# Performance work log

Measured on AMD Instinct MI355X. Metric: run time of the kernel, lower is better.

## Reference

```python
import jax, jax.numpy as jnp
import numpy as np


def setup_inputs() -> dict:
    key = jax.random.key(0)
    T, TOK, D = 16, 4096, 2048
    C = D // 2          # comp_dim
    H = 2 * C           # MLP hidden = comp_dim * 2
    K = 16              # comp_len
    NN = T * (TOK // 2)  # node rows == edge rows == 32768
    ks = jax.random.split(key, 10)
    x = jax.random.normal(ks[0], (T, TOK, D), dtype=jnp.float32)
    # structured ragged layout: first half of tokens are nodes, second half edges
    padded_node_mask = jnp.zeros((T, TOK), dtype=bool).at[:, :TOK // 2].set(True)
    padded_edge_mask = jnp.logical_not(padded_node_mask)
    rand_indices = jax.random.randint(ks[1], (2 * K, 1000), 0, NN)
    s = 0.02
    node_W1 = s * jax.random.normal(ks[2], (K, D, H), dtype=jnp.float32)
    node_b1 = jnp.zeros((K, H), dtype=jnp.float32)
    node_W2 = s * jax.random.normal(ks[3], (K, H, C), dtype=jnp.float32)
    node_b2 = jnp.zeros((K, C), dtype=jnp.float32)
    edge_W1 = s * jax.random.normal(ks[4], (K, D, H), dtype=jnp.float32)
    edge_b1 = jnp.zeros((K, H), dtype=jnp.float32)
    edge_W2 = s * jax.random.normal(ks[5], (K, H, C), dtype=jnp.float32)
    edge_b2 = jnp.zeros((K, C), dtype=jnp.float32)
    return {"x": x, "padded_node_mask": padded_node_mask,
            "padded_edge_mask": padded_edge_mask, "rand_indices": rand_indices,
            "node_W1": node_W1, "node_b1": node_b1, "node_W2": node_W2, "node_b2": node_b2,
            "edge_W1": edge_W1, "edge_b1": edge_b1, "edge_W2": edge_W2, "edge_b2": edge_b2}


def _branch(rows, seg, idx, W1, b1, W2, b2, T, TOK, NROWS, C):
    # rows: [NROWS, D] gathered tokens; seg: [NROWS] timestamp id per row
    # idx:  [K, 1000] sampled rows per component MLP
    sel = rows[idx]                                                # [K,1000,D]
    h = jax.nn.gelu(jnp.einsum('kld,kdh->klh', sel, W1) + b1[:, None, :],
                    approximate=False)
    h = jnp.einsum('klh,khc->klc', h, W2) + b2[:, None, :]         # [K,1000,C]

    def step(carry, args):
        i, hh = args
        # scatter-set dedupes duplicate sampled indices (same value anyway),
        # matching torch's zeros[...] = mlp(...) assignment semantics
        z = jnp.zeros((NROWS, C), dtype=hh.dtype).at[i].set(hh)    # sparse rows
        pooled = jax.ops.segment_sum(z, seg, num_segments=T)       # [T,C]
        return carry, pooled

    _, pooled = jax.lax.scan(step, None, (idx, h))                 # [K,T,C]
    # adaptive_avg_pool1d(..., 1) == mean over the full token dim (incl. zeros)
    return pooled / TOK


def reference(x, padded_node_mask, padded_edge_mask, rand_indices,
              node_W1, node_b1, node_W2, node_b2,
              edge_W1, edge_b1, edge_W2, edge_b2):
    T, TOK, D = x.shape
    C = D // 2
    K = node_W1.shape[0]
    NN = T * TOK // 2  # node rows (== edge rows for our structured masks)
    nt, ntok = jnp.nonzero(padded_node_mask, size=NN)
    et, etok = jnp.nonzero(padded_edge_mask, size=NN)
    nodes = x[nt, ntok]  # [NN, D], row-major order like torch x[mask]
    edges = x[et, etok]
    node_pooled = _branch(nodes, nt, rand_indices[:K],
                          node_W1, node_b1, node_W2, node_b2, T, TOK, NN, C)
    edge_pooled = _branch(edges, et, rand_indices[K:],
                          edge_W1, edge_b1, edge_W2, edge_b2, T, TOK, NN, C)
    comp = jnp.concatenate([node_pooled, edge_pooled], axis=0)     # [2K,T,C]
    # cat along feature dim in component order -> [T, 1, 2K*C]
    compressed_x = comp.transpose(1, 0, 2).reshape(T, 1, 2 * K * C)
    return compressed_x
```

## Files before the change

kernel.cpp:

```cpp
#include <hip/hip_runtime.h>
#include <math.h>


typedef __attribute__((ext_vector_type(8))) short bf16x8;
typedef __attribute__((ext_vector_type(4))) short s16x4;
typedef __attribute__((ext_vector_type(4))) float f32x4;
typedef unsigned int u32;

constexpr int TT    = 16;
constexpr int TOKN  = 4096;
constexpr int DD    = 2048;
constexpr int HH    = 2048;
constexpr int CC    = 1024;
constexpr int LL    = 1000;
constexpr int NCOMP = 32;
constexpr int MP    = 1024;
constexpr int BMX = 256, BNX = 128;
constexpr int MTX  = MP / BMX;
constexpr int NT1 = HH / BNX;
constexpr int NT2 = CC / BNX;
constexpr int NT  = 2048 / 64;

__device__ __forceinline__ short f2bf(float f) {
  __bf16 h = (__bf16)f;
  return *reinterpret_cast<short*>(&h);
}
__device__ __forceinline__ int swz(int row) {
  return (row & 7) ^ ((row >> 3) & 7);
}
__device__ __forceinline__ int sw(int row, int gran) {
  return (row << 6) + ((gran ^ swz(row)) << 3);
}
__device__ __forceinline__ void gl_lds16(const void* g, void* l) {
  __builtin_amdgcn_global_load_lds(
      (const __attribute__((address_space(1))) u32*)g,
      (__attribute__((address_space(3))) u32*)l, 16, 0, 0);
}

__global__ void dedup_kernel(const int* __restrict__ ridx,
                             unsigned* __restrict__ bitmap,
                             float* __restrict__ keepf) {
  int comp = blockIdx.x;
  for (int l = threadIdx.x; l < MP; l += 256) {
    float kv = 0.0f;
    if (l < LL) {
      int r = ridx[comp * LL + l];
      unsigned bit = 1u << (r & 31);
      unsigned old = atomicOr(&bitmap[(comp << 10) + (r >> 5)], bit);
      kv = (old & bit) ? 0.0f : 1.0f;
    }
    keepf[(comp << 10) + l] = kv;
  }
}

__global__ __launch_bounds__(256) void gather_kernel(
    const float* __restrict__ x, const int* __restrict__ ridx,
    short* __restrict__ Ab) {
  int bid = blockIdx.x;
  int comp = bid >> 7, rgrp = bid & 127;
  int t = threadIdx.x;
  int tr = t >> 5, tn = t & 31;
  int m = rgrp * 8 + tr;
  int mi = m < LL ? m : LL - 1;
  int r = ridx[comp * LL + mi];
  int tokoff = comp >= 16 ? TOKN / 2 : 0;
  const float* src = x + ((size_t)(r >> 11) * TOKN + (r & 2047) + tokoff) * DD;
  short* drow = Ab + ((size_t)(comp * MP + m)) * DD;
  int s_m = swz(m);
#pragma unroll
  for (int i = 0; i < 8; ++i) {
    int gi = tn + 32 * i;
    float4 f0 = *reinterpret_cast<const float4*>(src + gi * 8);
    float4 f1 = *reinterpret_cast<const float4*>(src + gi * 8 + 4);
    bf16x8 pk;
    pk[0]=f2bf(f0.x); pk[1]=f2bf(f0.y); pk[2]=f2bf(f0.z); pk[3]=f2bf(f0.w);
    pk[4]=f2bf(f1.x); pk[5]=f2bf(f1.y); pk[6]=f2bf(f1.z); pk[7]=f2bf(f1.w);
    int c = gi >> 3, g = gi & 7;
    *reinterpret_cast<bf16x8*>(&drow[c * 64 + ((g ^ s_m) << 3)]) = pk;
  }
}

template<int LDW>
__device__ __forceinline__ void kloop(
    const short* __restrict__ aBase,
    const float* __restrict__ wBase,
    short* sm, f32x4 (&acc)[8][4],
    int wm, int wn, int lr, int lg, int tid) {
  const short* aSrc0 = aBase + (size_t)(tid >> 3) * 2048 + (tid & 7) * 8;
  int ldsA0 = tid * 8;
  int tn = tid & 31, tkb = tid >> 5, bn0 = tn * 4;
  const float* wCol = wBase + bn0;

  float4 brB[8];

  auto aglds = [&](int t, int buf) {
    short* l = sm + buf * 16384;
#pragma unroll
    for (int q = 0; q < 8; ++q)
      gl_lds16(aSrc0 + (size_t)q * 65536 + t * 64, l + ldsA0 + q * 2048);
  };
  auto bload = [&](int t) {
    const float* bb = wCol + (size_t)(t * 64 + tkb * 8) * LDW;
#pragma unroll
    for (int i = 0; i < 8; ++i)
      brB[i] = *reinterpret_cast<const float4*>(bb + (size_t)i * LDW);
  };
  auto bwrite = [&]() {
    short* Bs = sm + 32768;
#pragma unroll
    for (int j = 0; j < 4; ++j) {
      bf16x8 pk;
#pragma unroll
      for (int i = 0; i < 8; ++i) pk[i] = f2bf((&brB[i].x)[j]);
      *reinterpret_cast<bf16x8*>(&Bs[sw(bn0 + j, tkb)]) = pk;
    }
  };
  auto compute = [&](int d) {
    const short* A = sm + d * 16384;
    const short* B = sm + 32768;
#pragma unroll
    for (int kk = 0; kk < 2; ++kk) {
      bf16x8 af[8], bfr[4];
#pragma unroll
      for (int i = 0; i < 8; ++i)
        af[i] = *reinterpret_cast<const bf16x8*>(&A[sw(wm + i * 16 + lr, kk * 4 + lg)]);
#pragma unroll
      for (int j = 0; j < 4; ++j)
        bfr[j] = *reinterpret_cast<const bf16x8*>(&B[sw(wn + j * 16 + lr, kk * 4 + lg)]);
      __builtin_amdgcn_s_setprio(1);
#pragma unroll
      for (int i = 0; i < 8; ++i)
#pragma unroll
        for (int j = 0; j < 4; ++j)
          acc[i][j] = __builtin_amdgcn_mfma_f32_16x16x32_bf16(af[i], bfr[j], acc[i][j], 0, 0, 0);
      __builtin_amdgcn_s_setprio(0);
    }
  };

  bload(0);
  aglds(0, 0);
  bwrite();
  bload(1);
  aglds(1, 1);
  asm volatile("s_waitcnt lgkmcnt(0)" ::: "memory");
  __builtin_amdgcn_s_barrier();

#pragma unroll 1
  for (int t = 0; t < NT; ++t) {
    if (t < NT - 1) {
      asm volatile("s_waitcnt vmcnt(16)" ::: "memory");
    } else {
      asm volatile("s_waitcnt vmcnt(0)" ::: "memory");
    }
    __builtin_amdgcn_sched_barrier(0);
    compute(t & 1);
    __builtin_amdgcn_s_barrier();
    if (t + 1 < NT) {
      bwrite();
      if (t + 2 < NT) {
        bload(t + 2);
        aglds(t + 2, t & 1);
      }
      asm volatile("s_waitcnt lgkmcnt(0)" ::: "memory");
      __builtin_amdgcn_s_barrier();
    }
  }
}

__global__ __launch_bounds__(256, 2) void gemm1_kernel(
    const float* __restrict__ nW1, const float* __restrict__ nb1,
    const float* __restrict__ eW1, const float* __restrict__ eb1,
    const short* __restrict__ Ab, short* __restrict__ hbuf) {
  __shared__ short smem[40960];

  constexpr int NWG = NCOMP * MTX * NT1;
  constexpr int CPX = NWG / 8;
  int b0 = blockIdx.x;
  int lb = (b0 & 7) * CPX + (b0 >> 3);
  int comp = lb / (MTX * NT1);
  int rem  = lb % (MTX * NT1);
  int mt = rem / NT1, nt = rem % NT1;
  bool isEdge = comp >= 16;
  int k16 = isEdge ? comp - 16 : comp;
  const float* W1 = (isEdge ? eW1 : nW1) + (size_t)k16 * DD * HH;
  const float* b1 = (isEdge ? eb1 : nb1) + (size_t)k16 * HH;

  int tid = threadIdx.x, lane = tid & 63, wid = tid >> 6;
  int wm = (wid >> 1) << 7, wn = (wid & 1) << 6;
  int lr = lane & 15, lg = lane >> 4;

  f32x4 acc[8][4] = {};
  kloop<HH>(Ab + ((size_t)(comp * MP + mt * BMX)) * DD,
            W1 + nt * BNX, smem, acc, wm, wn, lr, lg, tid);

  __builtin_amdgcn_s_barrier();
  short* Cs = smem;
  const float* b1p = b1 + nt * BNX;
#pragma unroll
  for (int i = 0; i < 8; ++i)
#pragma unroll
    for (int j = 0; j < 4; ++j) {
      int nl = wn + j * 16 + lr;
      float bias = b1p[nl];
#pragma unroll
      for (int rr = 0; rr < 4; ++rr) {
        int ml = wm + i * 16 + lg * 4 + rr;
        float v = acc[i][j][rr] + bias;
        float ge = 0.5f * v * (1.0f + erff(v * 0.70710678118654752f));
        Cs[ml * 132 + nl] = f2bf(ge);
      }
    }
  __syncthreads();
  short* hrow = hbuf + ((size_t)(comp * MP + mt * BMX)) * HH;
#pragma unroll
  for (int q = 0; q < 32; ++q) {
    int gl = q * 256 + tid;
    int r = gl >> 5, gg = gl & 31;
    s16x4 v = *reinterpret_cast<const s16x4*>(&Cs[r * 132 + gg * 4]);
    int dst = (nt * 2 + (gg >> 4)) * 64 + ((((gg >> 1) & 7) ^ swz(r)) << 3) + (gg & 1) * 4;
    *reinterpret_cast<s16x4*>(&hrow[(size_t)r * HH + dst]) = v;
  }
}

__global__ __launch_bounds__(256, 2) void gemm2_kernel(
    const short* __restrict__ hbuf, const int* __restrict__ ridx,
    const float* __restrict__ nW2, const float* __restrict__ nb2,
    const float* __restrict__ eW2, const float* __restrict__ eb2,
    const float* __restrict__ keepf, float* __restrict__ partial) {
  __shared__ short smem[40960];

  constexpr int NWG = NCOMP * MTX * NT2;
  constexpr int CPX = NWG / 8;
  int b0 = blockIdx.x;
  int lb = (b0 & 7) * CPX + (b0 >> 3);
  int comp = lb / (MTX * NT2);
  int rem  = lb % (MTX * NT2);
  int mt = rem / NT2, nt = rem % NT2;
  bool isEdge = comp >= 16;
  int k16 = isEdge ? comp - 16 : comp;
  const float* W2 = (isEdge ? eW2 : nW2) + (size_t)k16 * HH * CC;
  const float* b2 = (isEdge ? eb2 : nb2) + (size_t)k16 * CC;

  int tid = threadIdx.x, lane = tid & 63, wid = tid >> 6;
  int wm = (wid >> 1) << 7, wn = (wid & 1) << 6;
  int lr = lane & 15, lg = lane >> 4;

  f32x4 acc[8][4] = {};
  kloop<CC>(hbuf + ((size_t)(comp * MP + mt * BMX)) * HH,
            W2 + nt * BNX, smem, acc, wm, wn, lr, lg, tid);

  __builtin_amdgcn_s_barrier();
  float* part = (float*)smem;
  int*   tarr = (int*)((char*)smem + 8192);
  float* karr = (float*)((char*)smem + 9216);
  if (tid < BMX) {
    int mglob = mt * BMX + tid;
    int mi = mglob < LL ? mglob : LL - 1;
    int r2 = ridx[comp * LL + mi];
    tarr[tid] = r2 >> 11;
    karr[tid] = keepf[(comp << 10) + mglob];
  }
  for (int e = tid; e < TT * BNX; e += 256) part[e] = 0.0f;
  __syncthreads();
  const float* b2p = b2 + nt * BNX;
#pragma unroll
  for (int i = 0; i < 8; ++i)
#pragma unroll
    for (int j = 0; j < 4; ++j) {
      int nl = wn + j * 16 + lr;
      float bias = b2p[nl];
#pragma unroll
      for (int rr = 0; rr < 4; ++rr) {
        int ml = wm + i * 16 + lg * 4 + rr;
        float v = (acc[i][j][rr] + bias) * karr[ml];
        atomicAdd(&part[tarr[ml] * BNX + nl], v);
      }
    }
  __syncthreads();
  float* pout = partial + ((size_t)(comp * MTX + mt)) * TT * CC + nt * BNX;
  for (int e = tid; e < TT * BNX; e += 256) {
    int t2 = e >> 7, c = e & 127;
    pout[(size_t)t2 * CC + c] = part[e];
  }
}

__global__ void reduce_kernel(const float* __restrict__ partial,
                              float* __restrict__ out) {
  int idx = blockIdx.x * 256 + threadIdx.x;
  int c    = idx & (CC - 1);
  int comp = (idx >> 10) & (NCOMP - 1);
  int t    = idx >> 15;
  float s = 0.0f;
#pragma unroll
  for (int mt = 0; mt < MTX; ++mt)
    s += partial[(((size_t)(comp * MTX + mt)) * TT + t) * CC + c];
  out[idx] = s * (1.0f / 4096.0f);
}

extern "C" void kernel_launch(void* const* d_in, const int* in_sizes, int n_in,
                              void* d_out, int out_size, void* d_ws, size_t ws_size,
                              hipStream_t stream) {
  const float* x    = (const float*)d_in[0];
  const int*   ridx = (const int*)d_in[3];
  const float* nW1  = (const float*)d_in[4];
  const float* nb1  = (const float*)d_in[5];
  const float* nW2  = (const float*)d_in[6];
  const float* nb2  = (const float*)d_in[7];
  const float* eW1  = (const float*)d_in[8];
  const float* eb1  = (const float*)d_in[9];
  const float* eW2  = (const float*)d_in[10];
  const float* eb2  = (const float*)d_in[11];
  float* out = (float*)d_out;

  const size_t H_B   = (size_t)NCOMP * MP * HH * 2;
  const size_t BMP_B = (size_t)NCOMP * 1024 * 4;
  const size_t KP_B  = (size_t)NCOMP * 1024 * 4;
  const size_t PRT_B = (size_t)NCOMP * MTX * TT * CC * 4;
  const size_t base  = H_B + BMP_B + KP_B + PRT_B;

  char* ws = (char*)d_ws;
  short* hbuf      = (short*)ws;
  unsigned* bitmap = (unsigned*)(ws + H_B);
  float* keepf     = (float*)(ws + H_B + BMP_B);
  float* partial   = (float*)(ws + H_B + BMP_B + KP_B);
  short* Ab        = (short*)(ws + base);

  hipMemsetAsync(bitmap, 0, BMP_B, stream);
  dedup_kernel<<<NCOMP, 256, 0, stream>>>(ridx, bitmap, keepf);
  gather_kernel<<<NCOMP * 128, 256, 0, stream>>>(x, ridx, Ab);
  gemm1_kernel<<<NCOMP * MTX * NT1, 256, 0, stream>>>(nW1, nb1, eW1, eb1, Ab, hbuf);
  gemm2_kernel<<<NCOMP * MTX * NT2, 256, 0, stream>>>(hbuf, ridx, nW2, nb2, eW2, eb2, keepf, partial);
  reduce_kernel<<<out_size / 256, 256, 0, stream>>>(partial, out);
}
```

Measured before the change: 805.2 us.

## Use 256x256 tiles with 8 waves and interleaved ping-pong GEMM pipeline

Both grouped GEMMs move from 256x128 tiles with 4 waves to 256x256 tiles with 8 waves, with a new k-loop that double-buffers both A and B in LDS. The k-loop splits each tile into four MFMA quarter-phases, interleaving LDS fragment reads, global prefetch and bf16 B conversion with barriers. The aim is to halve the redundant A-tile traffic per output and overlap memory with MFMA work. In exchange, LDS use rises to 128KB per block, adding occupancy pressure, and the extra barriers and a two-pass GELU epilogue may add sync cost.

```diff
diff --git a/kernel.cpp b/kernel.cpp
--- a/kernel.cpp
+++ b/kernel.cpp
@@ -15,11 +15,11 @@
 constexpr int LL    = 1000;
 constexpr int NCOMP = 32;
 constexpr int MP    = 1024;
-constexpr int BMX = 256, BNX = 128;
+constexpr int BMX = 256, BNX = 256;
 constexpr int MTX  = MP / BMX;
-constexpr int NT1 = HH / BNX;
-constexpr int NT2 = CC / BNX;
-constexpr int NT  = 2048 / 64;
+constexpr int NT1X = HH / BNX;
+constexpr int NT2X = CC / BNX;
+constexpr int NT   = 2048 / 64;
 
 __device__ __forceinline__ short f2bf(float f) {
   __bf16 h = (__bf16)f;
@@ -81,205 +81,227 @@
 }
 
 template<int LDW>
-__device__ __forceinline__ void kloop(
+__device__ __forceinline__ void kloop8(
     const short* __restrict__ aBase,
     const float* __restrict__ wBase,
-    short* sm, f32x4 (&acc)[8][4],
-    int wm, int wn, int lr, int lg, int tid) {
+    short* sm, f32x4 (&acc)[8][4], int wr, int wc, int lr, int lg, int tid) {
   const short* aSrc0 = aBase + (size_t)(tid >> 3) * 2048 + (tid & 7) * 8;
   int ldsA0 = tid * 8;
-  int tn = tid & 31, tkb = tid >> 5, bn0 = tn * 4;
+  int tn = tid & 63, tkb = tid >> 6, bn0 = tn * 4;
   const float* wCol = wBase + bn0;
 
-  float4 brB[8];
-
-  auto aglds = [&](int t, int buf) {
-    short* l = sm + buf * 16384;
-#pragma unroll
-    for (int q = 0; q < 8; ++q)
-      gl_lds16(aSrc0 + (size_t)q * 65536 + t * 64, l + ldsA0 + q * 2048);
-  };
-  auto bload = [&](int t) {
-    const float* bb = wCol + (size_t)(t * 64 + tkb * 8) * LDW;
-#pragma unroll
-    for (int i = 0; i < 8; ++i)
-      brB[i] = *reinterpret_cast<const float4*>(bb + (size_t)i * LDW);
-  };
-  auto bwrite = [&]() {
-    short* Bs = sm + 32768;
+  float4 br[8];
+  bf16x8 af[2][4], bj0[2][2], bj1[2][2];
+
+  auto aglds = [&](int t) {
+    short* l = sm + (t & 1) * 16384;
+#pragma unroll
+    for (int q = 0; q < 4; ++q)
+      gl_lds16(aSrc0 + (size_t)q * 131072 + t * 64, l + ldsA0 + q * 4096);
+  };
+  auto bload4 = [&](int t, int h) {
+    const float* bb = wCol + (size_t)(t * 64 + tkb * 8 + h * 4) * LDW;
+#pragma unroll
+    for (int i = 0; i < 4; ++i)
+      br[h * 4 + i] = *reinterpret_cast<const float4*>(bb + (size_t)i * LDW);
+  };
+  auto bwrite4 = [&](int t, int h) {
+    short* Bs = sm + 32768 + (t & 1) * 16384;
 #pragma unroll
     for (int j = 0; j < 4; ++j) {
-      bf16x8 pk;
-#pragma unroll
-      for (int i = 0; i < 8; ++i) pk[i] = f2bf((&brB[i].x)[j]);
-      *reinterpret_cast<bf16x8*>(&Bs[sw(bn0 + j, tkb)]) = pk;
-    }
-  };
-  auto compute = [&](int d) {
-    const short* A = sm + d * 16384;
-    const short* B = sm + 32768;
-#pragma unroll
-    for (int kk = 0; kk < 2; ++kk) {
-      bf16x8 af[8], bfr[4];
-#pragma unroll
-      for (int i = 0; i < 8; ++i)
-        af[i] = *reinterpret_cast<const bf16x8*>(&A[sw(wm + i * 16 + lr, kk * 4 + lg)]);
-#pragma unroll
-      for (int j = 0; j < 4; ++j)
-        bfr[j] = *reinterpret_cast<const bf16x8*>(&B[sw(wn + j * 16 + lr, kk * 4 + lg)]);
-      __builtin_amdgcn_s_setprio(1);
-#pragma unroll
-      for (int i = 0; i < 8; ++i)
-#pragma unroll
-        for (int j = 0; j < 4; ++j)
-          acc[i][j] = __builtin_amdgcn_mfma_f32_16x16x32_bf16(af[i], bfr[j], acc[i][j], 0, 0, 0);
-      __builtin_amdgcn_s_setprio(0);
-    }
-  };
-
-  bload(0);
-  aglds(0, 0);
-  bwrite();
-  bload(1);
-  aglds(1, 1);
-  asm volatile("s_waitcnt lgkmcnt(0)" ::: "memory");
+      s16x4 pk;
+#pragma unroll
+      for (int i = 0; i < 4; ++i) pk[i] = f2bf((&br[h * 4 + i].x)[j]);
+      *reinterpret_cast<s16x4*>(&Bs[sw(bn0 + j, tkb) + h * 4]) = pk;
+    }
+  };
+  auto rdA = [&](int d, int qr) {
+#pragma unroll
+    for (int kk = 0; kk < 2; ++kk)
+#pragma unroll
+      for (int i = 0; i < 4; ++i)
+        af[kk][i] = *reinterpret_cast<const bf16x8*>(
+            &sm[d * 16384 + sw(wr * 128 + qr * 64 + i * 16 + lr, kk * 4 + lg)]);
+  };
+  auto rdB = [&](int d, int qc, bf16x8 (&bj)[2][2]) {
+#pragma unroll
+    for (int kk = 0; kk < 2; ++kk)
+#pragma unroll
+      for (int j = 0; j < 2; ++j)
+        bj[kk][j] = *reinterpret_cast<const bf16x8*>(
+            &sm[32768 + d * 16384 + sw(wc * 64 + qc * 32 + j * 16 + lr, kk * 4 + lg)]);
+  };
+  auto mfma16 = [&](bf16x8 (&bj)[2][2], int I0, int J0) {
+    __builtin_amdgcn_s_setprio(1);
+#pragma unroll
+    for (int kk = 0; kk < 2; ++kk)
+#pragma unroll
+      for (int i = 0; i < 4; ++i)
+#pragma unroll
+        for (int j = 0; j < 2; ++j)
+          acc[I0 + i][J0 + j] = __builtin_amdgcn_mfma_f32_16x16x32_bf16(
+              af[kk][i], bj[kk][j], acc[I0 + i][J0 + j], 0, 0, 0);
+    __builtin_amdgcn_s_setprio(0);
+  };
+
+  auto tile = [&](int t, bool stg) {
+    int d = t & 1;
+    rdA(d, 0); rdB(d, 0, bj0);
+    if (stg) { aglds(t + 1); bload4(t + 1, 0); }
+    __builtin_amdgcn_s_barrier();
+    asm volatile("s_waitcnt lgkmcnt(0)" ::: "memory");
+    mfma16(bj0, 0, 0);
+    __builtin_amdgcn_s_barrier();
+    rdB(d, 1, bj1);
+    if (stg) bload4(t + 1, 1);
+    __builtin_amdgcn_s_barrier();
+    asm volatile("s_waitcnt lgkmcnt(0)" ::: "memory");
+    mfma16(bj1, 0, 2);
+    __builtin_amdgcn_s_barrier();
+    rdA(d, 1);
+    if (stg) bwrite4(t + 1, 0);
+    __builtin_amdgcn_s_barrier();
+    asm volatile("s_waitcnt lgkmcnt(0)" ::: "memory");
+    mfma16(bj1, 4, 2);
+    __builtin_amdgcn_s_barrier();
+    if (stg) bwrite4(t + 1, 1);
+    __builtin_amdgcn_s_barrier();
+    asm volatile("s_waitcnt lgkmcnt(0)" ::: "memory");
+    mfma16(bj0, 4, 0);
+    __builtin_amdgcn_s_barrier();
+  };
+
+  aglds(0);
+  bload4(0, 0); bload4(0, 1);
+  bwrite4(0, 0); bwrite4(0, 1);
+  asm volatile("s_waitcnt vmcnt(0) lgkmcnt(0)" ::: "memory");
   __builtin_amdgcn_s_barrier();
 
 #pragma unroll 1
-  for (int t = 0; t < NT; ++t) {
-    if (t < NT - 1) {
-      asm volatile("s_waitcnt vmcnt(16)" ::: "memory");
-    } else {
-      asm volatile("s_waitcnt vmcnt(0)" ::: "memory");
-    }
-    __builtin_amdgcn_sched_barrier(0);
-    compute(t & 1);
-    __builtin_amdgcn_s_barrier();
-    if (t + 1 < NT) {
-      bwrite();
-      if (t + 2 < NT) {
-        bload(t + 2);
-        aglds(t + 2, t & 1);
-      }
-      asm volatile("s_waitcnt lgkmcnt(0)" ::: "memory");
-      __builtin_amdgcn_s_barrier();
-    }
-  }
-}
-
-__global__ __launch_bounds__(256, 2) void gemm1_kernel(
+  for (int tp = 0; tp < NT / 2; ++tp) {
+    tile(2 * tp, true);
+    tile(2 * tp + 1, tp < NT / 2 - 1);
+  }
+  __builtin_amdgcn_s_barrier();
+}
+
+__global__ __launch_bounds__(512, 2) void gemm1_kernel(
     const float* __restrict__ nW1, const float* __restrict__ nb1,
     const float* __restrict__ eW1, const float* __restrict__ eb1,
     const short* __restrict__ Ab, short* __restrict__ hbuf) {
-  __shared__ short smem[40960];
-
-  constexpr int NWG = NCOMP * MTX * NT1;
+  __shared__ short smem[65536];
+
+  constexpr int NWG = NCOMP * MTX * NT1X;
   constexpr int CPX = NWG / 8;
   int b0 = blockIdx.x;
   int lb = (b0 & 7) * CPX + (b0 >> 3);
-  int comp = lb / (MTX * NT1);
-  int rem  = lb % (MTX * NT1);
-  int mt = rem / NT1, nt = rem % NT1;
+  int comp = lb / (MTX * NT1X);
+  int rem  = lb % (MTX * NT1X);
+  int mt = rem / NT1X, nt = rem % NT1X;
   bool isEdge = comp >= 16;
   int k16 = isEdge ? comp - 16 : comp;
   const float* W1 = (isEdge ? eW1 : nW1) + (size_t)k16 * DD * HH;
   const float* b1 = (isEdge ? eb1 : nb1) + (size_t)k16 * HH;
 
   int tid = threadIdx.x, lane = tid & 63, wid = tid >> 6;
-  int wm = (wid >> 1) << 7, wn = (wid & 1) << 6;
+  int wr = wid >> 2, wc = wid & 3;
   int lr = lane & 15, lg = lane >> 4;
 
   f32x4 acc[8][4] = {};
-  kloop<HH>(Ab + ((size_t)(comp * MP + mt * BMX)) * DD,
-            W1 + nt * BNX, smem, acc, wm, wn, lr, lg, tid);
-
-  __builtin_amdgcn_s_barrier();
+  kloop8<HH>(Ab + ((size_t)(comp * MP + mt * BMX)) * DD,
+             W1 + nt * BNX, smem, acc, wr, wc, lr, lg, tid);
+
   short* Cs = smem;
   const float* b1p = b1 + nt * BNX;
-#pragma unroll
-  for (int i = 0; i < 8; ++i)
-#pragma unroll
-    for (int j = 0; j < 4; ++j) {
-      int nl = wn + j * 16 + lr;
-      float bias = b1p[nl];
-#pragma unroll
-      for (int rr = 0; rr < 4; ++rr) {
-        int ml = wm + i * 16 + lg * 4 + rr;
-        float v = acc[i][j][rr] + bias;
-        float ge = 0.5f * v * (1.0f + erff(v * 0.70710678118654752f));
-        Cs[ml * 132 + nl] = f2bf(ge);
-      }
-    }
-  __syncthreads();
-  short* hrow = hbuf + ((size_t)(comp * MP + mt * BMX)) * HH;
-#pragma unroll
-  for (int q = 0; q < 32; ++q) {
-    int gl = q * 256 + tid;
-    int r = gl >> 5, gg = gl & 31;
-    s16x4 v = *reinterpret_cast<const s16x4*>(&Cs[r * 132 + gg * 4]);
-    int dst = (nt * 2 + (gg >> 4)) * 64 + ((((gg >> 1) & 7) ^ swz(r)) << 3) + (gg & 1) * 4;
-    *reinterpret_cast<s16x4*>(&hrow[(size_t)r * HH + dst]) = v;
-  }
-}
-
-__global__ __launch_bounds__(256, 2) void gemm2_kernel(
+#pragma unroll 1
+  for (int p = 0; p < 2; ++p) {
+    if (wr == p) {
+#pragma unroll
+      for (int i = 0; i < 8; ++i)
+#pragma unroll
+        for (int j = 0; j < 4; ++j) {
+          int nl = wc * 64 + j * 16 + lr;
+          float bias = b1p[nl];
+#pragma unroll
+          for (int rr = 0; rr < 4; ++rr) {
+            int r = i * 16 + lg * 4 + rr;
+            float v = acc[i][j][rr] + bias;
+            float ge = 0.5f * v * (1.0f + erff(v * 0.70710678118654752f));
+            Cs[r * 264 + nl] = f2bf(ge);
+          }
+        }
+    }
+    __syncthreads();
+    short* hrow = hbuf + ((size_t)(comp * MP + mt * BMX + p * 128)) * HH;
+#pragma unroll
+    for (int q = 0; q < 8; ++q) {
+      int f = q * 512 + tid;
+      int r = f >> 5, g8 = f & 31;
+      bf16x8 v = *reinterpret_cast<const bf16x8*>(&Cs[r * 264 + g8 * 8]);
+      int dst = (nt * 4 + (g8 >> 3)) * 64 + (((g8 & 7) ^ swz(r)) << 3);
+      *reinterpret_cast<bf16x8*>(&hrow[(size_t)r * HH + dst]) = v;
+    }
+    __syncthreads();
+  }
+}
+
+__global__ __launch_bounds__(512, 2) void gemm2_kernel(
     const short* __restrict__ hbuf, const int* __restrict__ ridx,
     const float* __restrict__ nW2, const float* __restrict__ nb2,
     const float* __restrict__ eW2, const float* __restrict__ eb2,
     const float* __restrict__ keepf, float* __restrict__ partial) {
-  __shared__ short smem[40960];
-
-  constexpr int NWG = NCOMP * MTX * NT2;
+  __shared__ short smem[65536];
+
+  constexpr int NWG = NCOMP * MTX * NT2X;
   constexpr int CPX = NWG / 8;
   int b0 = blockIdx.x;
   int lb = (b0 & 7) * CPX + (b0 >> 3);
-  int comp = lb / (MTX * NT2);
-  int rem  = lb % (MTX * NT2);
-  int mt = rem / NT2, nt = rem % NT2;
+  int comp = lb / (MTX * NT2X);
+  int rem  = lb % (MTX * NT2X);
+  int mt = rem / NT2X, nt = rem % NT2X;
   bool isEdge = comp >= 16;
   int k16 = isEdge ? comp - 16 : comp;
   const float* W2 = (isEdge ? eW2 : nW2) + (size_t)k16 * HH * CC;
   const float* b2 = (isEdge ? eb2 : nb2) + (size_t)k16 * CC;
 
   int tid = threadIdx.x, lane = tid & 63, wid = tid >> 6;
-  int wm = (wid >> 1) << 7, wn = (wid & 1) << 6;
+  int wr = wid >> 2, wc = wid & 3;
   int lr = lane & 15, lg = lane >> 4;
 
   f32x4 acc[8][4] = {};
-  kloop<CC>(hbuf + ((size_t)(comp * MP + mt * BMX)) * HH,
-            W2 + nt * BNX, smem, acc, wm, wn, lr, lg, tid);
-
-  __builtin_amdgcn_s_barrier();
+  kloop8<CC>(hbuf + ((size_t)(comp * MP + mt * BMX)) * HH,
+             W2 + nt * BNX, smem, acc, wr, wc, lr, lg, tid);
+
   float* part = (float*)smem;
-  int*   tarr = (int*)((char*)smem + 8192);
-  float* karr = (float*)((char*)smem + 9216);
-  if (tid < BMX) {
+  int*   tarr = (int*)((char*)smem + 16384);
+  float* karr = (float*)((char*)smem + 17408);
+  if (tid < 256) {
     int mglob = mt * BMX + tid;
     int mi = mglob < LL ? mglob : LL - 1;
     int r2 = ridx[comp * LL + mi];
     tarr[tid] = r2 >> 11;
     karr[tid] = keepf[(comp << 10) + mglob];
   }
-  for (int e = tid; e < TT * BNX; e += 256) part[e] = 0.0f;
+  for (int e = tid; e < TT * 256; e += 512) part[e] = 0.0f;
   __syncthreads();
   const float* b2p = b2 + nt * BNX;
 #pragma unroll
   for (int i = 0; i < 8; ++i)
 #pragma unroll
     for (int j = 0; j < 4; ++j) {
-      int nl = wn + j * 16 + lr;
+      int nl = wc * 64 + j * 16 + lr;
       float bias = b2p[nl];
 #pragma unroll
       for (int rr = 0; rr < 4; ++rr) {
-        int ml = wm + i * 16 + lg * 4 + rr;
+        int ml = wr * 128 + i * 16 + lg * 4 + rr;
         float v = (acc[i][j][rr] + bias) * karr[ml];
-        atomicAdd(&part[tarr[ml] * BNX + nl], v);
+        atomicAdd(&part[tarr[ml] * 256 + nl], v);
       }
     }
   __syncthreads();
   float* pout = partial + ((size_t)(comp * MTX + mt)) * TT * CC + nt * BNX;
-  for (int e = tid; e < TT * BNX; e += 256) {
-    int t2 = e >> 7, c = e & 127;
+  for (int e = tid; e < TT * 256; e += 512) {
+    int t2 = e >> 8, c = e & 255;
     pout[(size_t)t2 * CC + c] = part[e];
   }
 }
@@ -328,7 +350,7 @@
   hipMemsetAsync(bitmap, 0, BMP_B, stream);
   dedup_kernel<<<NCOMP, 256, 0, stream>>>(ridx, bitmap, keepf);
   gather_kernel<<<NCOMP * 128, 256, 0, stream>>>(x, ridx, Ab);
-  gemm1_kernel<<<NCOMP * MTX * NT1, 256, 0, stream>>>(nW1, nb1, eW1, eb1, Ab, hbuf);
-  gemm2_kernel<<<NCOMP * MTX * NT2, 256, 0, stream>>>(hbuf, ridx, nW2, nb2, eW2, eb2, keepf, partial);
+  gemm1_kernel<<<NCOMP * MTX * NT1X, 512, 0, stream>>>(nW1, nb1, eW1, eb1, Ab, hbuf);
+  gemm2_kernel<<<NCOMP * MTX * NT2X, 512, 0, stream>>>(hbuf, ridx, nW2, nb2, eW2, eb2, keepf, partial);
   reduce_kernel<<<out_size / 256, 256, 0, stream>>>(partial, out);
 }
```

Result: slower. 1.225 ms (+52.1%).

## Deepen weight prefetch pipeline and pad LDS partial-sum rows in gemm2 epilogue

Applied to the files above, without the earlier changes.

The shared GEMM k-loop now splits the fp32 weight load from its bf16 conversion. Loads are issued three tiles ahead and converted one tile ahead into registers, so the LDS store after the barrier is a plain write, and the vmcnt waits are retuned to match. The sched_barrier is also removed. Separately, the gemm2 epilogue pads its per-timestamp partial-sum rows to 257 floats so atomics to different timestamps land in different LDS banks. The deeper prefetch keeps more VGPRs live (raw float4 loads plus packed bf16), which may pressure occupancy at 2 waves per SIMD. Removing the sched barrier may also let the compiler reorder the waits.

```diff
diff --git a/kernel.cpp b/kernel.cpp
--- a/kernel.cpp
+++ b/kernel.cpp
@@ -91,7 +91,8 @@
   int tn = tid & 31, tkb = tid >> 5, bn0 = tn * 4;
   const float* wCol = wBase + bn0;
 
-  float4 brB[8];
+  float4  br[8];
+  bf16x8  bb[4];
 
   auto aglds = [&](int t, int buf) {
     short* l = sm + buf * 16384;
@@ -100,20 +101,25 @@
       gl_lds16(aSrc0 + (size_t)q * 65536 + t * 64, l + ldsA0 + q * 2048);
   };
   auto bload = [&](int t) {
-    const float* bb = wCol + (size_t)(t * 64 + tkb * 8) * LDW;
+    const float* bb_ = wCol + (size_t)(t * 64 + tkb * 8) * LDW;
 #pragma unroll
     for (int i = 0; i < 8; ++i)
-      brB[i] = *reinterpret_cast<const float4*>(bb + (size_t)i * LDW);
+      br[i] = *reinterpret_cast<const float4*>(bb_ + (size_t)i * LDW);
+  };
+  auto bcvt = [&]() {
+#pragma unroll
+    for (int j = 0; j < 4; ++j) {
+      bf16x8 pk;
+#pragma unroll
+      for (int i = 0; i < 8; ++i) pk[i] = f2bf((&br[i].x)[j]);
+      bb[j] = pk;
+    }
   };
   auto bwrite = [&]() {
     short* Bs = sm + 32768;
 #pragma unroll
-    for (int j = 0; j < 4; ++j) {
-      bf16x8 pk;
-#pragma unroll
-      for (int i = 0; i < 8; ++i) pk[i] = f2bf((&brB[i].x)[j]);
-      *reinterpret_cast<bf16x8*>(&Bs[sw(bn0 + j, tkb)]) = pk;
-    }
+    for (int j = 0; j < 4; ++j)
+      *reinterpret_cast<bf16x8*>(&Bs[sw(bn0 + j, tkb)]) = bb[j];
   };
   auto compute = [&](int d) {
     const short* A = sm + d * 16384;
@@ -138,31 +144,36 @@
   };
 
   bload(0);
+  bcvt();
+  bwrite();
   aglds(0, 0);
-  bwrite();
   bload(1);
+  bcvt();
+  bload(2);
   aglds(1, 1);
   asm volatile("s_waitcnt lgkmcnt(0)" ::: "memory");
   __builtin_amdgcn_s_barrier();
 
 #pragma unroll 1
-  for (int t = 0; t < NT; ++t) {
-    if (t < NT - 1) {
+  for (int u = 0; u < NT; ++u) {
+    if (u < NT - 2) {
       asm volatile("s_waitcnt vmcnt(16)" ::: "memory");
+    } else if (u == NT - 2) {
+      asm volatile("s_waitcnt vmcnt(8)" ::: "memory");
     } else {
       asm volatile("s_waitcnt vmcnt(0)" ::: "memory");
     }
-    __builtin_amdgcn_sched_barrier(0);
-    compute(t & 1);
+    compute(u & 1);
     __builtin_amdgcn_s_barrier();
-    if (t + 1 < NT) {
+    if (u + 1 < NT) {
       bwrite();
-      if (t + 2 < NT) {
-        bload(t + 2);
-        aglds(t + 2, t & 1);
-      }
       asm volatile("s_waitcnt lgkmcnt(0)" ::: "memory");
-      __builtin_amdgcn_s_barrier();
+    }
+    __builtin_amdgcn_s_barrier();
+    if (u + 2 < NT) {
+      bcvt();
+      if (u + 3 < NT) bload(u + 3);
+      aglds(u + 2, u & 1);
     }
   }
 }
@@ -251,8 +262,8 @@
 
   __builtin_amdgcn_s_barrier();
   float* part = (float*)smem;
-  int*   tarr = (int*)((char*)smem + 8192);
-  float* karr = (float*)((char*)smem + 9216);
+  int*   tarr = (int*)((char*)smem + 16640);
+  float* karr = (float*)((char*)smem + 17664);
   if (tid < BMX) {
     int mglob = mt * BMX + tid;
     int mi = mglob < LL ? mglob : LL - 1;
@@ -260,7 +271,7 @@
     tarr[tid] = r2 >> 11;
     karr[tid] = keepf[(comp << 10) + mglob];
   }
-  for (int e = tid; e < TT * BNX; e += 256) part[e] = 0.0f;
+  for (int e = tid; e < TT * 257; e += 256) part[e] = 0.0f;
   __syncthreads();
   const float* b2p = b2 + nt * BNX;
 #pragma unroll
@@ -273,14 +284,14 @@
       for (int rr = 0; rr < 4; ++rr) {
         int ml = wm + i * 16 + lg * 4 + rr;
         float v = (acc[i][j][rr] + bias) * karr[ml];
-        atomicAdd(&part[tarr[ml] * BNX + nl], v);
+        atomicAdd(&part[tarr[ml] * 257 + nl], v);
       }
     }
   __syncthreads();
   float* pout = partial + ((size_t)(comp * MTX + mt)) * TT * CC + nt * BNX;
   for (int e = tid; e < TT * BNX; e += 256) {
     int t2 = e >> 7, c = e & 127;
-    pout[(size_t)t2 * CC + c] = part[e];
+    pout[(size_t)t2 * CC + c] = part[t2 * 257 + c];
   }
 }
 
```

Result: slower. 919.9 us (+14.2%).
